# Kernel tuning notes

Hardware: AMD Instinct MI355X
Metric: run time of the kernel (lower is better)

## Reference

```python
import jax, jax.numpy as jnp
import numpy as np

N_NODES = 20000
N_EDGES = 640000
NODE_NF = 64
HIDDEN = 256
N_LAYERS = 4


def _linear_init(key, fan_in, fan_out, layers=None):
    shape = (fan_in, fan_out) if layers is None else (layers, fan_in, fan_out)
    scale = 1.0 / np.sqrt(fan_in)
    return jax.random.normal(key, shape, dtype=jnp.float32) * scale


def setup_inputs() -> dict:
    key = jax.random.key(0)
    ks = jax.random.split(key, 16)
    L, H = N_LAYERS, HIDDEN
    return {
        "h": jax.random.normal(ks[0], (N_NODES, NODE_NF), dtype=jnp.float32),
        "edge_index": jax.random.randint(ks[1], (2, N_EDGES), 0, N_NODES, dtype=jnp.int64),
        "coord_diff": jax.random.normal(ks[2], (N_EDGES, 3), dtype=jnp.float32),
        # embedding in / out
        "w_in": _linear_init(ks[3], NODE_NF, H),
        "b_in": jnp.zeros((H,), jnp.float32),
        "w_out": _linear_init(ks[4], H, NODE_NF),
        "b_out": jnp.zeros((NODE_NF,), jnp.float32),
        # per-layer edge MLP: Linear(2H+1 -> H), silu, Linear(H -> H), silu
        "edge_w1": _linear_init(ks[5], 2 * H + 1, H, L),
        "edge_b1": jnp.zeros((L, H), jnp.float32),
        "edge_w2": _linear_init(ks[6], H, H, L),
        "edge_b2": jnp.zeros((L, H), jnp.float32),
        # per-layer node MLP: Linear(2H -> H), silu, Linear(H -> H)
        "node_w1": _linear_init(ks[7], 2 * H, H, L),
        "node_b1": jnp.zeros((L, H), jnp.float32),
        "node_w2": _linear_init(ks[8], H, H, L),
        "node_b2": jnp.zeros((L, H), jnp.float32),
    }


def reference(h, edge_index, coord_diff, w_in, b_in, w_out, b_out,
              edge_w1, edge_b1, edge_w2, edge_b2,
              node_w1, node_b1, node_w2, node_b2):
    row, col = edge_index[0], edge_index[1]
    # radial is layer-independent: [E, 1]
    radial = jnp.sum(coord_diff ** 2, axis=1, keepdims=True)

    h = h @ w_in + b_in  # [N, H]
    n_nodes = h.shape[0]

    for l in range(N_LAYERS):
        # edge model: gather endpoints, concat with radial, 2-layer MLP
        m = jnp.concatenate([h[row], h[col], radial], axis=1)  # [E, 2H+1]
        m = jax.nn.silu(m @ edge_w1[l] + edge_b1[l])
        m = jax.nn.silu(m @ edge_w2[l] + edge_b2[l])  # [E, H]
        # node model: segment-sum aggregate over row, concat, 2-layer MLP
        agg = jax.ops.segment_sum(m, row, num_segments=n_nodes)  # [N, H]
        x = jnp.concatenate([h, agg], axis=1)  # [N, 2H]
        x = jax.nn.silu(x @ node_w1[l] + node_b1[l])
        h = x @ node_w2[l] + node_b2[l]  # recurrent=False: no residual

    return h @ w_out + b_out  # [N, node_nf]
```

## Files before the change

### kernel.cpp

```cpp
#include <hip/hip_runtime.h>
#include <hip/hip_bf16.h>
#include <cstdint>
#include <cstddef>

#define NN 20000
#define NE 640000
#define NF 64
#define HD 256
#define NL 4
#define HTS 640

typedef __attribute__((ext_vector_type(8))) short short8;
typedef __attribute__((ext_vector_type(4))) float f32x4;
typedef __attribute__((ext_vector_type(2))) float f32x2;

__device__ __forceinline__ float bf2f(unsigned short u){
  union { unsigned int i; float f; } x; x.i = ((unsigned int)u) << 16; return x.f;
}
__device__ __forceinline__ unsigned short f2bf(float f){
  union { float f; unsigned int i; } x; x.f = f;
  unsigned int r = x.i + 0x7FFFu + ((x.i >> 16) & 1u);
  return (unsigned short)(r >> 16);
}
__device__ __forceinline__ unsigned int pk2bf(float a, float b){
  union { __hip_bfloat162 h; unsigned int u; } cv;
  cv.h = __float22bfloat162_rn(float2{a, b});
  return cv.u;
}
__device__ __forceinline__ float silu_f(float v){
  float e = __builtin_amdgcn_exp2f(v * -1.442695041f);
  return v * __builtin_amdgcn_rcpf(1.0f + e);
}
__device__ __forceinline__ f32x2 silu2(f32x2 v){
  f32x2 t = v * (f32x2){-1.442695041f, -1.442695041f};
  f32x2 e = (f32x2){__builtin_amdgcn_exp2f(t.x), __builtin_amdgcn_exp2f(t.y)};
  f32x2 d = e + (f32x2){1.0f, 1.0f};
  f32x2 r = (f32x2){__builtin_amdgcn_rcpf(d.x), __builtin_amdgcn_rcpf(d.y)};
  return v * r;
}
__device__ __forceinline__ void async16(const void* g, void* l){
  __builtin_amdgcn_global_load_lds(
      (const __attribute__((address_space(1))) unsigned int*)g,
      (__attribute__((address_space(3))) unsigned int*)l, 16, 0, 0);
}

__global__ __launch_bounds__(256) void prep_small(
    const float* __restrict__ w_in, const float* __restrict__ w_out,
    const float* __restrict__ ew1, const float* __restrict__ ew2,
    const float* __restrict__ nw1, const float* __restrict__ nw2,
    const float* __restrict__ eb1,
    unsigned short* __restrict__ w_in_t, unsigned short* __restrict__ w_out_t,
    unsigned short* __restrict__ ew1cat, float* __restrict__ w1r,
    float* __restrict__ b1e,
    unsigned short* __restrict__ ew2t, unsigned short* __restrict__ nw1t,
    unsigned short* __restrict__ nw2t)
{
  const int s = blockIdx.y;
  const int tid = blockIdx.x * 256 + threadIdx.x;
  if (s == 18) {
    if (tid < NL * 512) {
      int l = tid >> 9, c = tid & 511;
      b1e[tid] = (c < 256) ? eb1[l * HD + c] : 0.0f;
    }
    return;
  }
  if (s >= 2 && s < 6) {
    int l = s - 2;
    if (tid >= 513 * HD) return;
    int k = tid / HD, n = tid - k * HD;
    float v = ew1[(size_t)l * 513 * HD + tid];
    if (k == 512) { w1r[l * HD + n] = v; return; }
    unsigned short* dst = ew1cat + (size_t)l * 512 * 256;
    if (k < 256) dst[(size_t)n * 256 + k] = f2bf(v);
    else         dst[(size_t)(256 + n) * 256 + (k - 256)] = f2bf(v);
    return;
  }
  const float* src; unsigned short* dst; int K, N;
  if (s == 0)      { src = w_in;  dst = w_in_t;  K = NF;   N = HD; }
  else if (s == 1) { src = w_out; dst = w_out_t; K = HD;   N = NF; }
  else if (s < 10) { int l = s-6;  src = ew2 + (size_t)l*HD*HD;   dst = ew2t + (size_t)l*HD*HD;  K = HD;   N = HD; }
  else if (s < 14) { int l = s-10; src = nw1 + (size_t)l*2*HD*HD; dst = nw1t + (size_t)l*HD*512; K = 2*HD; N = HD; }
  else             { int l = s-14; src = nw2 + (size_t)l*HD*HD;   dst = nw2t + (size_t)l*HD*HD;  K = HD;   N = HD; }
  if (tid >= K * N) return;
  int k = tid / N, n = tid - k * N;
  dst[(size_t)n * K + k] = f2bf(src[tid]);
}

__global__ __launch_bounds__(256) void prep_big(
    const float* __restrict__ h_in, const float* __restrict__ cd,
    unsigned short* __restrict__ hb_in, float* __restrict__ radial)
{
  const int s = blockIdx.y;
  const int tid = blockIdx.x * 256 + threadIdx.x;
  if (s == 0) {
    if (tid < NN * NF) hb_in[tid] = f2bf(h_in[tid]);
  } else {
    if (tid < NE) {
      float x = cd[tid*3+0], y = cd[tid*3+1], z = cd[tid*3+2];
      radial[tid] = x*x + y*y + z*z;
    }
  }
}

__global__ __launch_bounds__(256) void hist_k(const int* __restrict__ erow, int* __restrict__ hist){
  int e = blockIdx.x * 256 + threadIdx.x;
  if (e < NE){
    unsigned r = (unsigned)erow[e]; if (r >= NN) r = 0;
    atomicAdd(&hist[r], 1);
  }
}

__global__ __launch_bounds__(256) void scan_k(const int* __restrict__ hist,
                                              int* __restrict__ starts, int* __restrict__ cursor){
  __shared__ int part[256];
  const int t = threadIdx.x;
  const int CH = 79;
  int lo = t * CH, hi = lo + CH; if (hi > NN) hi = NN; if (lo > NN) lo = NN;
  int s = 0;
  for (int i = lo; i < hi; ++i) s += hist[i];
  part[t] = s; __syncthreads();
  for (int off = 1; off < 256; off <<= 1){
    int v = (t >= off) ? part[t - off] : 0;
    __syncthreads();
    part[t] += v;
    __syncthreads();
  }
  int base = (t == 0) ? 0 : part[t - 1];
  for (int i = lo; i < hi; ++i){ starts[i] = base; cursor[i] = base; base += hist[i]; }
  if (t == 255) starts[NN] = part[255];
}

__global__ __launch_bounds__(256) void scatter_k(const int* __restrict__ erow,
                                                 const int* __restrict__ ecol,
                                                 const float* __restrict__ radial,
                                                 int* __restrict__ cursor,
                                                 int* __restrict__ rowcol,
                                                 float* __restrict__ radial_s){
  int e = blockIdx.x * 256 + threadIdx.x;
  if (e < NE){
    unsigned r = (unsigned)erow[e]; if (r >= NN) r = 0;
    unsigned c = (unsigned)ecol[e]; if (c >= NN) c = 0;
    int pos = atomicAdd(&cursor[r], 1);
    rowcol[2*pos]   = (int)r;
    rowcol[2*pos+1] = (int)c;
    radial_s[pos] = radial[e];
  }
}

__global__ __launch_bounds__(256, 4) void node0_k(
    const unsigned short* __restrict__ hb,
    const unsigned short* __restrict__ w_in_t,
    const float* __restrict__ b_in,
    const unsigned short* __restrict__ w1cat0,
    const float* __restrict__ b1e0,
    unsigned short* __restrict__ hcur,
    unsigned short* __restrict__ hT,
    int M)
{
  __shared__ __align__(16) unsigned short As[32*64];
  __shared__ __align__(16) unsigned short Bs[256*32];
  __shared__ __align__(16) unsigned short xL[8*32*32];
  const int t = threadIdx.x;
  const int lane = t & 63, wave = t >> 6;
  const int ln15 = lane & 15, q = lane >> 4;
  const int bm = blockIdx.x;
  const int sc = (t & 3) * 8;
  const int srB = t >> 2;

  float bvin[4];
  #pragma unroll
  for (int j = 0; j < 4; ++j) bvin[j] = b_in[wave*64 + j*16 + ln15];

  f32x4 acc[2][4];
  #pragma unroll
  for (int i = 0; i < 2; ++i)
    #pragma unroll
    for (int j = 0; j < 4; ++j) acc[i][j] = (f32x4){0.f,0.f,0.f,0.f};

  async16(hb + (size_t)(bm*32 + (t >> 3)) * NF + (t & 7)*8, &As[t*8]);

  for (int kt = 0; kt < 2; ++kt) {
    #pragma unroll
    for (int i = 0; i < 4; ++i)
      async16(w_in_t + (size_t)(i*64 + srB) * NF + kt*32 + sc, &Bs[i*2048 + t*8]);
    __syncthreads();
    short8 fa[2], fb[4];
    #pragma unroll
    for (int i = 0; i < 2; ++i) fa[i] = *(const short8*)&As[(i*16 + ln15)*64 + kt*32 + q*8];
    #pragma unroll
    for (int j = 0; j < 4; ++j) fb[j] = *(const short8*)&Bs[(wave*64 + j*16 + ln15)*32 + q*8];
    #pragma unroll
    for (int i = 0; i < 2; ++i)
      #pragma unroll
      for (int j = 0; j < 4; ++j)
        acc[i][j] = __builtin_amdgcn_mfma_f32_16x16x32_bf16(fa[i], fb[j], acc[i][j], 0, 0, 0);
    __syncthreads();
  }

  #pragma unroll
  for (int i = 0; i < 2; ++i) {
    #pragma unroll
    for (int j = 0; j < 4; ++j) {
      const int n = wave*64 + j*16 + ln15;
      const int kt2 = n >> 5, k31 = n & 31;
      const int r0 = i*16 + q*4;
      const int m0 = bm*32 + r0;
      #pragma unroll
      for (int r = 0; r < 4; ++r) {
        unsigned short h = f2bf(acc[i][j][r] + bvin[j]);
        hcur[(size_t)(m0 + r) * HD + n] = h;
        xL[kt2*1024 + (r0 + r)*32 + k31] = h;
      }
    }
  }

  #pragma unroll
  for (int half = 0; half < 2; ++half) {
    #pragma unroll
    for (int i = 0; i < 2; ++i)
      #pragma unroll
      for (int j = 0; j < 4; ++j) acc[i][j] = (f32x4){0.f,0.f,0.f,0.f};
    for (int kt2 = 0; kt2 < 8; ++kt2) {
      #pragma unroll
      for (int i = 0; i < 4; ++i)
        async16(w1cat0 + (size_t)(half*256 + i*64 + srB) * 256 + kt2*32 + sc,
                &Bs[i*2048 + t*8]);
      __syncthreads();
      short8 fa[2], fb[4];
      #pragma unroll
      for (int i = 0; i < 2; ++i) fa[i] = *(const short8*)&xL[kt2*1024 + (i*16 + ln15)*32 + q*8];
      #pragma unroll
      for (int j = 0; j < 4; ++j) fb[j] = *(const short8*)&Bs[(wave*64 + j*16 + ln15)*32 + q*8];
      #pragma unroll
      for (int i = 0; i < 2; ++i)
        #pragma unroll
        for (int j = 0; j < 4; ++j)
          acc[i][j] = __builtin_amdgcn_mfma_f32_16x16x32_bf16(fa[i], fb[j], acc[i][j], 0, 0, 0);
      __syncthreads();
    }
    #pragma unroll
    for (int i = 0; i < 2; ++i) {
      #pragma unroll
      for (int j = 0; j < 4; ++j) {
        const int n = half*256 + wave*64 + j*16 + ln15;
        const float bv = b1e0[n];
        #pragma unroll
        for (int r = 0; r < 4; ++r) {
          const int m = bm*32 + i*16 + q*4 + r;
          hT[(size_t)m * HTS + n] = f2bf(acc[i][j][r] + bv);
        }
      }
    }
  }
  (void)M;
}

__global__ __launch_bounds__(256, 4) void node_k(
    unsigned short* __restrict__ hcur,
    float* __restrict__ aggF,
    const unsigned short* __restrict__ w1t,
    const float* __restrict__ b1,
    const unsigned short* __restrict__ w2t,
    const float* __restrict__ b2,
    const unsigned short* __restrict__ w1cat_next,
    const float* __restrict__ b1e_next,
    unsigned short* __restrict__ hT,
    const unsigned short* __restrict__ w_out_t,
    const float* __restrict__ b_out,
    float* __restrict__ outF,
    int M)
{
  __shared__ __align__(16) unsigned short As[32*32];
  __shared__ __align__(16) unsigned short Bs[256*32];
  __shared__ __align__(16) unsigned short xL[8*32*32];
  const int t = threadIdx.x;
  const int lane = t & 63, wave = t >> 6;
  const int ln15 = lane & 15, q = lane >> 4;
  const int bm = blockIdx.x;
  const int sc = (t & 3) * 8;
  const int srA = (t & 127) >> 2;
  const int srB = t >> 2;

  const int rowA = bm*32 + srA;
  const unsigned short* aSrc = hcur + (size_t)rowA * HD + sc;
  float* gSrc = aggF + (size_t)rowA * HD + sc;

  float bv1[4], bv2[4];
  #pragma unroll
  for (int j = 0; j < 4; ++j) {
    bv1[j] = b1[wave*64 + j*16 + ln15];
    bv2[j] = b2[wave*64 + j*16 + ln15];
  }

  f32x4 acc[2][4];
  #pragma unroll
  for (int i = 0; i < 2; ++i)
    #pragma unroll
    for (int j = 0; j < 4; ++j) acc[i][j] = (f32x4){0.f,0.f,0.f,0.f};

  for (int kt = 0; kt < 16; ++kt) {
    if (t < 128) {
      if (kt < 8) {
        async16(aSrc + kt*32, &As[t*8]);
      } else {
        float* p = gSrc + (kt-8)*32;
        float4 a0 = *(const float4*)p;
        float4 a1 = *(const float4*)(p + 4);
        union { unsigned int u[4]; short8 s8; } cv;
        cv.u[0] = pk2bf(a0.x, a0.y); cv.u[1] = pk2bf(a0.z, a0.w);
        cv.u[2] = pk2bf(a1.x, a1.y); cv.u[3] = pk2bf(a1.z, a1.w);
        *(float4*)p = float4{0.f,0.f,0.f,0.f};
        *(float4*)(p + 4) = float4{0.f,0.f,0.f,0.f};
        *(short8*)&As[t*8] = cv.s8;
      }
    }
    #pragma unroll
    for (int i = 0; i < 4; ++i)
      async16(w1t + (size_t)(i*64 + srB) * 512 + kt*32 + sc, &Bs[i*2048 + t*8]);
    __syncthreads();
    short8 fa[2], fb[4];
    #pragma unroll
    for (int i = 0; i < 2; ++i) fa[i] = *(const short8*)&As[(i*16 + ln15)*32 + q*8];
    #pragma unroll
    for (int j = 0; j < 4; ++j) fb[j] = *(const short8*)&Bs[(wave*64 + j*16 + ln15)*32 + q*8];
    #pragma unroll
    for (int i = 0; i < 2; ++i)
      #pragma unroll
      for (int j = 0; j < 4; ++j)
        acc[i][j] = __builtin_amdgcn_mfma_f32_16x16x32_bf16(fa[i], fb[j], acc[i][j], 0, 0, 0);
    __syncthreads();
  }

  #pragma unroll
  for (int i = 0; i < 2; ++i) {
    #pragma unroll
    for (int j = 0; j < 4; ++j) {
      const int k = wave*64 + j*16 + ln15;
      const int kt2 = k >> 5, k31 = k & 31;
      const f32x2 bb = (f32x2){bv1[j], bv1[j]};
      f32x2 s01 = (f32x2){acc[i][j][0], acc[i][j][1]} + bb;
      f32x2 s23 = (f32x2){acc[i][j][2], acc[i][j][3]} + bb;
      f32x2 r01 = silu2(s01);
      f32x2 r23 = silu2(s23);
      const int r0 = i*16 + q*4;
      xL[kt2*1024 + (r0  )*32 + k31] = f2bf(r01.x);
      xL[kt2*1024 + (r0+1)*32 + k31] = f2bf(r01.y);
      xL[kt2*1024 + (r0+2)*32 + k31] = f2bf(r23.x);
      xL[kt2*1024 + (r0+3)*32 + k31] = f2bf(r23.y);
    }
  }
  #pragma unroll
  for (int i = 0; i < 2; ++i)
    #pragma unroll
    for (int j = 0; j < 4; ++j) acc[i][j] = (f32x4){0.f,0.f,0.f,0.f};

  for (int kt2 = 0; kt2 < 8; ++kt2) {
    #pragma unroll
    for (int i = 0; i < 4; ++i)
      async16(w2t + (size_t)(i*64 + srB) * 256 + kt2*32 + sc, &Bs[i*2048 + t*8]);
    __syncthreads();
    short8 fa[2], fb[4];
    #pragma unroll
    for (int i = 0; i < 2; ++i) fa[i] = *(const short8*)&xL[kt2*1024 + (i*16 + ln15)*32 + q*8];
    #pragma unroll
    for (int j = 0; j < 4; ++j) fb[j] = *(const short8*)&Bs[(wave*64 + j*16 + ln15)*32 + q*8];
    #pragma unroll
    for (int i = 0; i < 2; ++i)
      #pragma unroll
      for (int j = 0; j < 4; ++j)
        acc[i][j] = __builtin_amdgcn_mfma_f32_16x16x32_bf16(fa[i], fb[j], acc[i][j], 0, 0, 0);
    __syncthreads();
  }

  #pragma unroll
  for (int i = 0; i < 2; ++i) {
    #pragma unroll
    for (int j = 0; j < 4; ++j) {
      const int n = wave*64 + j*16 + ln15;
      const int kt2 = n >> 5, k31 = n & 31;
      const int r0 = i*16 + q*4;
      const int m0 = bm*32 + r0;
      #pragma unroll
      for (int r = 0; r < 4; ++r) {
        unsigned short h = f2bf(acc[i][j][r] + bv2[j]);
        hcur[(size_t)(m0 + r) * HD + n] = h;
        xL[kt2*1024 + (r0 + r)*32 + k31] = h;
      }
    }
  }

  if (w1cat_next) {
    #pragma unroll
    for (int half = 0; half < 2; ++half) {
      #pragma unroll
      for (int i = 0; i < 2; ++i)
        #pragma unroll
        for (int j = 0; j < 4; ++j) acc[i][j] = (f32x4){0.f,0.f,0.f,0.f};
      for (int kt2 = 0; kt2 < 8; ++kt2) {
        #pragma unroll
        for (int i = 0; i < 4; ++i)
          async16(w1cat_next + (size_t)(half*256 + i*64 + srB) * 256 + kt2*32 + sc,
                  &Bs[i*2048 + t*8]);
        __syncthreads();
        short8 fa[2], fb[4];
        #pragma unroll
        for (int i = 0; i < 2; ++i) fa[i] = *(const short8*)&xL[kt2*1024 + (i*16 + ln15)*32 + q*8];
        #pragma unroll
        for (int j = 0; j < 4; ++j) fb[j] = *(const short8*)&Bs[(wave*64 + j*16 + ln15)*32 + q*8];
        #pragma unroll
        for (int i = 0; i < 2; ++i)
          #pragma unroll
          for (int j = 0; j < 4; ++j)
            acc[i][j] = __builtin_amdgcn_mfma_f32_16x16x32_bf16(fa[i], fb[j], acc[i][j], 0, 0, 0);
        __syncthreads();
      }
      #pragma unroll
      for (int i = 0; i < 2; ++i) {
        #pragma unroll
        for (int j = 0; j < 4; ++j) {
          const int n = half*256 + wave*64 + j*16 + ln15;
          const float bv = b1e_next[n];
          #pragma unroll
          for (int r = 0; r < 4; ++r) {
            const int m = bm*32 + i*16 + q*4 + r;
            hT[(size_t)m * HTS + n] = f2bf(acc[i][j][r] + bv);
          }
        }
      }
    }
  } else {
    const int nD = wave*16 + ln15;
    const float bvD = b_out[nD];
    f32x4 accD[2];
    accD[0] = (f32x4){0.f,0.f,0.f,0.f};
    accD[1] = (f32x4){0.f,0.f,0.f,0.f};
    for (int kt2 = 0; kt2 < 8; ++kt2) {
      async16(w_out_t + (size_t)srB * 256 + kt2*32 + sc, &Bs[t*8]);
      __syncthreads();
      short8 fa[2], fb;
      #pragma unroll
      for (int i = 0; i < 2; ++i) fa[i] = *(const short8*)&xL[kt2*1024 + (i*16 + ln15)*32 + q*8];
      fb = *(const short8*)&Bs[nD*32 + q*8];
      #pragma unroll
      for (int i = 0; i < 2; ++i)
        accD[i] = __builtin_amdgcn_mfma_f32_16x16x32_bf16(fa[i], fb, accD[i], 0, 0, 0);
      __syncthreads();
    }
    #pragma unroll
    for (int i = 0; i < 2; ++i) {
      #pragma unroll
      for (int r = 0; r < 4; ++r) {
        const int m = bm*32 + i*16 + q*4 + r;
        outF[(size_t)m * NF + nD] = accD[i][r] + bvD;
      }
    }
  }
  (void)M;
}

__global__ __launch_bounds__(256, 4) void edge_k(
    const unsigned short* __restrict__ hT,
    const int* __restrict__ rowcol,
    const float* __restrict__ radial_s,
    const float* __restrict__ w1r,
    const unsigned short* __restrict__ w2t,
    const float* __restrict__ b2,
    float* __restrict__ agg)
{
  __shared__ __align__(16) unsigned short MBUF[16896];
  __shared__ int   rowS[64];
  __shared__ float w1rS[256];
  unsigned short* M1  = MBUF;
  unsigned short* m2T = MBUF;

  const int t = threadIdx.x;
  const int lane = t & 63, wave = t >> 6;
  const int ln15 = lane & 15, q = lane >> 4;
  int blk = blockIdx.x;
  blk = (blk & 7) * ((int)gridDim.x >> 3) + (blk >> 3);
  const int e0 = blk * 64;
  const int sr = t >> 2;
  const int sc_swz = (((t & 3) ^ ((sr >> 1) & 3))) * 8;
  const int xq = ((q ^ ((ln15 >> 1) & 3))) * 8;

  const int2 rc = *(const int2*)(rowcol + 2*(e0 + sr));
  int rowv = 0;
  if (t < 64) rowv = rowcol[2*(e0 + t)];
  const float w1v = w1r[t];
  const float rad = radial_s[e0 + sr];

  float bv2[4];
  #pragma unroll
  for (int j = 0; j < 4; ++j) bv2[j] = b2[wave*64 + j*16 + ln15];

  const unsigned short* hr = hT + (size_t)rc.x * HTS + sc_swz;
  const unsigned short* hc = hT + (size_t)rc.y * HTS + 256 + sc_swz;

  short8 va[8], vb[8];
  #pragma unroll
  for (int ch = 0; ch < 8; ++ch) {
    va[ch] = *(const short8*)(hr + ch*32);
    vb[ch] = *(const short8*)(hc + ch*32);
  }

  if (t < 64) rowS[t] = rowv;
  w1rS[t] = w1v;

  const unsigned short* w2row[4];
  #pragma unroll
  for (int j = 0; j < 4; ++j)
    w2row[j] = w2t + (size_t)(wave*64 + j*16 + ln15) * HD + q*8;

  __syncthreads();

  const f32x2 rad2 = (f32x2){rad, rad};
  #pragma unroll
  for (int ch = 0; ch < 8; ++ch) {
    const int c0 = ch*32 + sc_swz;
    const unsigned int* ua = (const unsigned int*)&va[ch];
    const unsigned int* ub = (const unsigned int*)&vb[ch];
    union { unsigned int u[4]; short8 s; } res;
    #pragma unroll
    for (int i = 0; i < 4; ++i) {
      union { unsigned int i; float f; } alo, ahi, blo, bhi;
      alo.i = ua[i] << 16; ahi.i = ua[i] & 0xFFFF0000u;
      blo.i = ub[i] << 16; bhi.i = ub[i] & 0xFFFF0000u;
      f32x2 av = (f32x2){alo.f, ahi.f};
      f32x2 bv = (f32x2){blo.f, bhi.f};
      f32x2 wv = *(const f32x2*)&w1rS[c0 + 2*i];
      f32x2 o = av + bv;
      o = o + rad2 * wv;
      f32x2 sv = silu2(o);
      res.u[i] = pk2bf(sv.x, sv.y);
    }
    *(short8*)&M1[ch*2048 + sr*32 + (t & 3)*8] = res.s;
  }
  __syncthreads();

  f32x4 acc2[4][4];
  #pragma unroll
  for (int i = 0; i < 4; ++i)
    #pragma unroll
    for (int j = 0; j < 4; ++j) acc2[i][j] = (f32x4){0.f,0.f,0.f,0.f};

  __builtin_amdgcn_s_setprio(1);
  #pragma unroll
  for (int kt = 0; kt < 8; ++kt) {
    short8 fa[4], fb[4];
    #pragma unroll
    for (int j = 0; j < 4; ++j) fb[j] = *(const short8*)(w2row[j] + kt*32);
    #pragma unroll
    for (int i = 0; i < 4; ++i) fa[i] = *(const short8*)&M1[kt*2048 + (i*16 + ln15)*32 + xq];
    #pragma unroll
    for (int i = 0; i < 4; ++i)
      #pragma unroll
      for (int j = 0; j < 4; ++j)
        acc2[i][j] = __builtin_amdgcn_mfma_f32_16x16x32_bf16(fa[i], fb[j], acc2[i][j], 0, 0, 0);
  }
  __builtin_amdgcn_s_setprio(0);
  __syncthreads();

  #pragma unroll
  for (int i = 0; i < 4; ++i) {
    #pragma unroll
    for (int j = 0; j < 4; ++j) {
      const int n = wave*64 + j*16 + ln15;
      const f32x2 b2v = (f32x2){bv2[j], bv2[j]};
      f32x2 s01 = (f32x2){acc2[i][j][0], acc2[i][j][1]} + b2v;
      f32x2 s23 = (f32x2){acc2[i][j][2], acc2[i][j][3]} + b2v;
      f32x2 r01 = silu2(s01);
      f32x2 r23 = silu2(s23);
      const int m = i*16 + q*4;
      *(unsigned int*)&m2T[n*66 + m]     = pk2bf(r01.x, r01.y);
      *(unsigned int*)&m2T[n*66 + m + 2] = pk2bf(r23.x, r23.y);
    }
  }
  __syncthreads();

  {
    const int c = t;
    int cur = __builtin_amdgcn_readfirstlane(rowS[0]);
    float s = 0.f;
    #pragma unroll
    for (int m = 0; m < 64; m += 4) {
      unsigned int u0 = *(const unsigned int*)&m2T[c*66 + m];
      unsigned int u1 = *(const unsigned int*)&m2T[c*66 + m + 2];
      int n0 = __builtin_amdgcn_readfirstlane(rowS[m]);
      int n1 = __builtin_amdgcn_readfirstlane(rowS[m+1]);
      int n2 = __builtin_amdgcn_readfirstlane(rowS[m+2]);
      int n3 = __builtin_amdgcn_readfirstlane(rowS[m+3]);
      float f0 = bf2f((unsigned short)u0), f1 = bf2f((unsigned short)(u0 >> 16));
      float f2v = bf2f((unsigned short)u1), f3 = bf2f((unsigned short)(u1 >> 16));
      if (n0 != cur) { atomicAdd(&agg[(size_t)cur * HD + c], s); s = 0.f; cur = n0; }
      s += f0;
      if (n1 != cur) { atomicAdd(&agg[(size_t)cur * HD + c], s); s = 0.f; cur = n1; }
      s += f1;
      if (n2 != cur) { atomicAdd(&agg[(size_t)cur * HD + c], s); s = 0.f; cur = n2; }
      s += f2v;
      if (n3 != cur) { atomicAdd(&agg[(size_t)cur * HD + c], s); s = 0.f; cur = n3; }
      s += f3;
    }
    atomicAdd(&agg[(size_t)cur * HD + c], s);
  }
}

extern "C" void kernel_launch(void* const* d_in, const int* in_sizes, int n_in,
                              void* d_out, int out_size, void* d_ws, size_t ws_size,
                              hipStream_t stream)
{
  (void)in_sizes; (void)n_in; (void)out_size; (void)ws_size;
  const float* h_in  = (const float*)d_in[0];
  const int*   ei    = (const int*)d_in[1];
  const float* cd    = (const float*)d_in[2];
  const float* w_in  = (const float*)d_in[3];
  const float* b_in  = (const float*)d_in[4];
  const float* w_out = (const float*)d_in[5];
  const float* b_out = (const float*)d_in[6];
  const float* ew1   = (const float*)d_in[7];
  const float* eb1   = (const float*)d_in[8];
  const float* ew2   = (const float*)d_in[9];
  const float* eb2   = (const float*)d_in[10];
  const float* nw1   = (const float*)d_in[11];
  const float* nb1   = (const float*)d_in[12];
  const float* nw2   = (const float*)d_in[13];
  const float* nb2   = (const float*)d_in[14];
  float* out = (float*)d_out;

  char* base = (char*)d_ws;
  size_t off = 0;
  auto WS = [&](size_t bytes) -> char* {
    char* p = base + off;
    off = (off + bytes + 255) & ~(size_t)255;
    return p;
  };
  float*          radial  = (float*)WS((size_t)NE * 4);
  unsigned short* hb_in   = (unsigned short*)WS((size_t)NN * NF * 2);
  unsigned short* hcur    = (unsigned short*)WS((size_t)NN * HD * 2);
  float*          aggF    = (float*)WS((size_t)NN * HD * 4);
  unsigned short* hT      = (unsigned short*)WS((size_t)NN * HTS * 2);
  unsigned short* w_in_t  = (unsigned short*)WS((size_t)NF * HD * 2);
  unsigned short* w_out_t = (unsigned short*)WS((size_t)NF * HD * 2);
  unsigned short* ew1cat  = (unsigned short*)WS((size_t)NL * 512 * 256 * 2);
  float*          w1r     = (float*)WS((size_t)NL * HD * 4);
  float*          b1e     = (float*)WS((size_t)NL * 512 * 4);
  unsigned short* ew2t    = (unsigned short*)WS((size_t)NL * HD * HD * 2);
  unsigned short* nw1t    = (unsigned short*)WS((size_t)NL * HD * 512 * 2);
  unsigned short* nw2t    = (unsigned short*)WS((size_t)NL * HD * HD * 2);
  int*            hist    = (int*)WS((size_t)NN * 4);
  int*            starts  = (int*)WS((size_t)(NN + 1) * 4);
  int*            cursor  = (int*)WS((size_t)NN * 4);
  int*            rowcol  = (int*)WS((size_t)NE * 2 * 4);
  float*          radial_s= (float*)WS((size_t)NE * 4);

  hipMemsetAsync(hist, 0, (size_t)NN * 4, stream);
  hipMemsetAsync(aggF, 0, (size_t)NN * HD * 4, stream);
  prep_small<<<dim3(513, 19), 256, 0, stream>>>(w_in, w_out, ew1, ew2, nw1, nw2, eb1,
      w_in_t, w_out_t, ew1cat, w1r, b1e, ew2t, nw1t, nw2t);
  prep_big<<<dim3(5000, 2), 256, 0, stream>>>(h_in, cd, hb_in, radial);
  hist_k<<<NE / 256, 256, 0, stream>>>(ei, hist);
  scan_k<<<1, 256, 0, stream>>>(hist, starts, cursor);
  scatter_k<<<NE / 256, 256, 0, stream>>>(ei, ei + NE, radial, cursor, rowcol, radial_s);

  node0_k<<<NN / 32, 256, 0, stream>>>(hb_in, w_in_t, b_in, ew1cat, b1e, hcur, hT, NN);

  for (int l = 0; l < NL; ++l) {
    edge_k<<<NE / 64, 256, 0, stream>>>(hT, rowcol, radial_s,
        w1r + l * HD, ew2t + (size_t)l * HD * HD, eb2 + l * HD, aggF);
    const int last = (l == NL - 1);
    node_k<<<NN / 32, 256, 0, stream>>>(hcur, aggF,
        nw1t + (size_t)l * HD * 512, nb1 + l * HD,
        nw2t + (size_t)l * HD * HD, nb2 + l * HD,
        last ? nullptr : (ew1cat + (size_t)(l+1) * 512 * 256),
        last ? nullptr : (b1e + (size_t)(l+1) * 512),
        hT, w_out_t, b_out, out, NN);
  }
}
```

Measured before the change: 1.146 ms.

## Halve node-kernel row tile to 16 and parallelize the CSR prefix scan

The node kernels (node0_k, node_k) now process 16 rows per block instead of 32, doubling the grid from 625 to 1250 blocks so more CUs stay busy on the 20000-node GEMMs. The price is that each block reloads the full weight tiles for half as many rows, which doubles weight traffic from L2. The single-block serial histogram scan is replaced by a three-kernel block-parallel scan (block sums, scan of sums, per-block scan). This removes a long serial step but adds two launches.

```diff
diff --git a/kernel.cpp b/kernel.cpp
--- a/kernel.cpp
+++ b/kernel.cpp
@@ -9,6 +9,8 @@
 #define HD 256
 #define NL 4
 #define HTS 640
+#define SR 16
+#define NB 79
 
 typedef __attribute__((ext_vector_type(8))) short short8;
 typedef __attribute__((ext_vector_type(4))) float f32x4;
@@ -110,24 +112,50 @@
   }
 }
 
-__global__ __launch_bounds__(256) void scan_k(const int* __restrict__ hist,
-                                              int* __restrict__ starts, int* __restrict__ cursor){
+__global__ __launch_bounds__(256) void scan1_k(const int* __restrict__ hist, int* __restrict__ bsum){
+  __shared__ int red[256];
+  const int t = threadIdx.x;
+  const int bin = blockIdx.x * 256 + t;
+  red[t] = (bin < NN) ? hist[bin] : 0;
+  __syncthreads();
+  for (int off = 128; off > 0; off >>= 1){
+    if (t < off) red[t] += red[t + off];
+    __syncthreads();
+  }
+  if (t == 0) bsum[blockIdx.x] = red[0];
+}
+
+__global__ __launch_bounds__(256) void scan2_k(const int* __restrict__ bsum, int* __restrict__ boff){
   __shared__ int part[256];
   const int t = threadIdx.x;
-  const int CH = 79;
-  int lo = t * CH, hi = lo + CH; if (hi > NN) hi = NN; if (lo > NN) lo = NN;
-  int s = 0;
-  for (int i = lo; i < hi; ++i) s += hist[i];
-  part[t] = s; __syncthreads();
+  int v = (t < NB) ? bsum[t] : 0;
+  part[t] = v;
+  __syncthreads();
   for (int off = 1; off < 256; off <<= 1){
-    int v = (t >= off) ? part[t - off] : 0;
-    __syncthreads();
-    part[t] += v;
-    __syncthreads();
-  }
-  int base = (t == 0) ? 0 : part[t - 1];
-  for (int i = lo; i < hi; ++i){ starts[i] = base; cursor[i] = base; base += hist[i]; }
-  if (t == 255) starts[NN] = part[255];
+    int p = (t >= off) ? part[t - off] : 0;
+    __syncthreads();
+    part[t] += p;
+    __syncthreads();
+  }
+  if (t < NB) boff[t] = part[t] - v;
+}
+
+__global__ __launch_bounds__(256) void scan3_k(const int* __restrict__ hist,
+                                               const int* __restrict__ boff,
+                                               int* __restrict__ cursor){
+  __shared__ int part[256];
+  const int t = threadIdx.x;
+  const int bin = blockIdx.x * 256 + t;
+  int v = (bin < NN) ? hist[bin] : 0;
+  part[t] = v;
+  __syncthreads();
+  for (int off = 1; off < 256; off <<= 1){
+    int p = (t >= off) ? part[t - off] : 0;
+    __syncthreads();
+    part[t] += p;
+    __syncthreads();
+  }
+  if (bin < NN) cursor[bin] = boff[blockIdx.x] + part[t] - v;
 }
 
 __global__ __launch_bounds__(256) void scatter_k(const int* __restrict__ erow,
@@ -154,12 +182,11 @@
     const unsigned short* __restrict__ w1cat0,
     const float* __restrict__ b1e0,
     unsigned short* __restrict__ hcur,
-    unsigned short* __restrict__ hT,
-    int M)
+    unsigned short* __restrict__ hT)
 {
-  __shared__ __align__(16) unsigned short As[32*64];
+  __shared__ __align__(16) unsigned short As[SR*64];
   __shared__ __align__(16) unsigned short Bs[256*32];
-  __shared__ __align__(16) unsigned short xL[8*32*32];
+  __shared__ __align__(16) unsigned short xL[8*SR*32];
   const int t = threadIdx.x;
   const int lane = t & 63, wave = t >> 6;
   const int ln15 = lane & 15, q = lane >> 4;
@@ -171,88 +198,72 @@
   #pragma unroll
   for (int j = 0; j < 4; ++j) bvin[j] = b_in[wave*64 + j*16 + ln15];
 
-  f32x4 acc[2][4];
-  #pragma unroll
-  for (int i = 0; i < 2; ++i)
-    #pragma unroll
-    for (int j = 0; j < 4; ++j) acc[i][j] = (f32x4){0.f,0.f,0.f,0.f};
-
-  async16(hb + (size_t)(bm*32 + (t >> 3)) * NF + (t & 7)*8, &As[t*8]);
+  f32x4 acc[4];
+  #pragma unroll
+  for (int j = 0; j < 4; ++j) acc[j] = (f32x4){0.f,0.f,0.f,0.f};
+
+  if (t < 128)
+    async16(hb + (size_t)(bm*SR + (t >> 3)) * NF + (t & 7)*8, &As[t*8]);
 
   for (int kt = 0; kt < 2; ++kt) {
     #pragma unroll
     for (int i = 0; i < 4; ++i)
       async16(w_in_t + (size_t)(i*64 + srB) * NF + kt*32 + sc, &Bs[i*2048 + t*8]);
     __syncthreads();
-    short8 fa[2], fb[4];
-    #pragma unroll
-    for (int i = 0; i < 2; ++i) fa[i] = *(const short8*)&As[(i*16 + ln15)*64 + kt*32 + q*8];
+    short8 fa, fb[4];
+    fa = *(const short8*)&As[ln15*64 + kt*32 + q*8];
     #pragma unroll
     for (int j = 0; j < 4; ++j) fb[j] = *(const short8*)&Bs[(wave*64 + j*16 + ln15)*32 + q*8];
     #pragma unroll
-    for (int i = 0; i < 2; ++i)
-      #pragma unroll
-      for (int j = 0; j < 4; ++j)
-        acc[i][j] = __builtin_amdgcn_mfma_f32_16x16x32_bf16(fa[i], fb[j], acc[i][j], 0, 0, 0);
-    __syncthreads();
-  }
-
-  #pragma unroll
-  for (int i = 0; i < 2; ++i) {
-    #pragma unroll
-    for (int j = 0; j < 4; ++j) {
-      const int n = wave*64 + j*16 + ln15;
-      const int kt2 = n >> 5, k31 = n & 31;
-      const int r0 = i*16 + q*4;
-      const int m0 = bm*32 + r0;
-      #pragma unroll
-      for (int r = 0; r < 4; ++r) {
-        unsigned short h = f2bf(acc[i][j][r] + bvin[j]);
-        hcur[(size_t)(m0 + r) * HD + n] = h;
-        xL[kt2*1024 + (r0 + r)*32 + k31] = h;
-      }
+    for (int j = 0; j < 4; ++j)
+      acc[j] = __builtin_amdgcn_mfma_f32_16x16x32_bf16(fa, fb[j], acc[j], 0, 0, 0);
+    __syncthreads();
+  }
+
+  #pragma unroll
+  for (int j = 0; j < 4; ++j) {
+    const int n = wave*64 + j*16 + ln15;
+    const int kt2 = n >> 5, k31 = n & 31;
+    const int r0 = q*4;
+    const int m0 = bm*SR + r0;
+    #pragma unroll
+    for (int r = 0; r < 4; ++r) {
+      unsigned short h = f2bf(acc[j][r] + bvin[j]);
+      hcur[(size_t)(m0 + r) * HD + n] = h;
+      xL[kt2*512 + (r0 + r)*32 + k31] = h;
     }
   }
 
   #pragma unroll
   for (int half = 0; half < 2; ++half) {
     #pragma unroll
-    for (int i = 0; i < 2; ++i)
-      #pragma unroll
-      for (int j = 0; j < 4; ++j) acc[i][j] = (f32x4){0.f,0.f,0.f,0.f};
+    for (int j = 0; j < 4; ++j) acc[j] = (f32x4){0.f,0.f,0.f,0.f};
     for (int kt2 = 0; kt2 < 8; ++kt2) {
       #pragma unroll
       for (int i = 0; i < 4; ++i)
         async16(w1cat0 + (size_t)(half*256 + i*64 + srB) * 256 + kt2*32 + sc,
                 &Bs[i*2048 + t*8]);
       __syncthreads();
-      short8 fa[2], fb[4];
-      #pragma unroll
-      for (int i = 0; i < 2; ++i) fa[i] = *(const short8*)&xL[kt2*1024 + (i*16 + ln15)*32 + q*8];
+      short8 fa, fb[4];
+      fa = *(const short8*)&xL[kt2*512 + ln15*32 + q*8];
       #pragma unroll
       for (int j = 0; j < 4; ++j) fb[j] = *(const short8*)&Bs[(wave*64 + j*16 + ln15)*32 + q*8];
       #pragma unroll
-      for (int i = 0; i < 2; ++i)
-        #pragma unroll
-        for (int j = 0; j < 4; ++j)
-          acc[i][j] = __builtin_amdgcn_mfma_f32_16x16x32_bf16(fa[i], fb[j], acc[i][j], 0, 0, 0);
+      for (int j = 0; j < 4; ++j)
+        acc[j] = __builtin_amdgcn_mfma_f32_16x16x32_bf16(fa, fb[j], acc[j], 0, 0, 0);
       __syncthreads();
     }
     #pragma unroll
-    for (int i = 0; i < 2; ++i) {
+    for (int j = 0; j < 4; ++j) {
+      const int n = half*256 + wave*64 + j*16 + ln15;
+      const float bv = b1e0[n];
       #pragma unroll
-      for (int j = 0; j < 4; ++j) {
-        const int n = half*256 + wave*64 + j*16 + ln15;
-        const float bv = b1e0[n];
-        #pragma unroll
-        for (int r = 0; r < 4; ++r) {
-          const int m = bm*32 + i*16 + q*4 + r;
-          hT[(size_t)m * HTS + n] = f2bf(acc[i][j][r] + bv);
-        }
+      for (int r = 0; r < 4; ++r) {
+        const int m = bm*SR + q*4 + r;
+        hT[(size_t)m * HTS + n] = f2bf(acc[j][r] + bv);
       }
     }
   }
-  (void)M;
 }
 
 __global__ __launch_bounds__(256, 4) void node_k(
@@ -267,21 +278,20 @@
     unsigned short* __restrict__ hT,
     const unsigned short* __restrict__ w_out_t,
     const float* __restrict__ b_out,
-    float* __restrict__ outF,
-    int M)
+    float* __restrict__ outF)
 {
-  __shared__ __align__(16) unsigned short As[32*32];
+  __shared__ __align__(16) unsigned short As[SR*32];
   __shared__ __align__(16) unsigned short Bs[256*32];
-  __shared__ __align__(16) unsigned short xL[8*32*32];
+  __shared__ __align__(16) unsigned short xL[8*SR*32];
   const int t = threadIdx.x;
   const int lane = t & 63, wave = t >> 6;
   const int ln15 = lane & 15, q = lane >> 4;
   const int bm = blockIdx.x;
   const int sc = (t & 3) * 8;
-  const int srA = (t & 127) >> 2;
+  const int srA = (t & 63) >> 2;
   const int srB = t >> 2;
 
-  const int rowA = bm*32 + srA;
+  const int rowA = bm*SR + srA;
   const unsigned short* aSrc = hcur + (size_t)rowA * HD + sc;
   float* gSrc = aggF + (size_t)rowA * HD + sc;
 
@@ -292,14 +302,12 @@
     bv2[j] = b2[wave*64 + j*16 + ln15];
   }
 
-  f32x4 acc[2][4];
-  #pragma unroll
-  for (int i = 0; i < 2; ++i)
-    #pragma unroll
-    for (int j = 0; j < 4; ++j) acc[i][j] = (f32x4){0.f,0.f,0.f,0.f};
+  f32x4 acc[4];
+  #pragma unroll
+  for (int j = 0; j < 4; ++j) acc[j] = (f32x4){0.f,0.f,0.f,0.f};
 
   for (int kt = 0; kt < 16; ++kt) {
-    if (t < 128) {
+    if (t < 64) {
       if (kt < 8) {
         async16(aSrc + kt*32, &As[t*8]);
       } else {
@@ -318,74 +326,60 @@
     for (int i = 0; i < 4; ++i)
       async16(w1t + (size_t)(i*64 + srB) * 512 + kt*32 + sc, &Bs[i*2048 + t*8]);
     __syncthreads();
-    short8 fa[2], fb[4];
-    #pragma unroll
-    for (int i = 0; i < 2; ++i) fa[i] = *(const short8*)&As[(i*16 + ln15)*32 + q*8];
+    short8 fa, fb[4];
+    fa = *(const short8*)&As[ln15*32 + q*8];
     #pragma unroll
     for (int j = 0; j < 4; ++j) fb[j] = *(const short8*)&Bs[(wave*64 + j*16 + ln15)*32 + q*8];
     #pragma unroll
-    for (int i = 0; i < 2; ++i)
-      #pragma unroll
-      for (int j = 0; j < 4; ++j)
-        acc[i][j] = __builtin_amdgcn_mfma_f32_16x16x32_bf16(fa[i], fb[j], acc[i][j], 0, 0, 0);
-    __syncthreads();
-  }
-
-  #pragma unroll
-  for (int i = 0; i < 2; ++i) {
-    #pragma unroll
-    for (int j = 0; j < 4; ++j) {
-      const int k = wave*64 + j*16 + ln15;
-      const int kt2 = k >> 5, k31 = k & 31;
-      const f32x2 bb = (f32x2){bv1[j], bv1[j]};
-      f32x2 s01 = (f32x2){acc[i][j][0], acc[i][j][1]} + bb;
-      f32x2 s23 = (f32x2){acc[i][j][2], acc[i][j][3]} + bb;
-      f32x2 r01 = silu2(s01);
-      f32x2 r23 = silu2(s23);
-      const int r0 = i*16 + q*4;
-      xL[kt2*1024 + (r0  )*32 + k31] = f2bf(r01.x);
-      xL[kt2*1024 + (r0+1)*32 + k31] = f2bf(r01.y);
-      xL[kt2*1024 + (r0+2)*32 + k31] = f2bf(r23.x);
-      xL[kt2*1024 + (r0+3)*32 + k31] = f2bf(r23.y);
-    }
-  }
-  #pragma unroll
-  for (int i = 0; i < 2; ++i)
-    #pragma unroll
-    for (int j = 0; j < 4; ++j) acc[i][j] = (f32x4){0.f,0.f,0.f,0.f};
+    for (int j = 0; j < 4; ++j)
+      acc[j] = __builtin_amdgcn_mfma_f32_16x16x32_bf16(fa, fb[j], acc[j], 0, 0, 0);
+    __syncthreads();
+  }
+
+  #pragma unroll
+  for (int j = 0; j < 4; ++j) {
+    const int k = wave*64 + j*16 + ln15;
+    const int kt2 = k >> 5, k31 = k & 31;
+    const f32x2 bb = (f32x2){bv1[j], bv1[j]};
+    f32x2 s01 = (f32x2){acc[j][0], acc[j][1]} + bb;
+    f32x2 s23 = (f32x2){acc[j][2], acc[j][3]} + bb;
+    f32x2 r01 = silu2(s01);
+    f32x2 r23 = silu2(s23);
+    const int r0 = q*4;
+    xL[kt2*512 + (r0  )*32 + k31] = f2bf(r01.x);
+    xL[kt2*512 + (r0+1)*32 + k31] = f2bf(r01.y);
+    xL[kt2*512 + (r0+2)*32 + k31] = f2bf(r23.x);
+    xL[kt2*512 + (r0+3)*32 + k31] = f2bf(r23.y);
+  }
+  #pragma unroll
+  for (int j = 0; j < 4; ++j) acc[j] = (f32x4){0.f,0.f,0.f,0.f};
 
   for (int kt2 = 0; kt2 < 8; ++kt2) {
     #pragma unroll
     for (int i = 0; i < 4; ++i)
       async16(w2t + (size_t)(i*64 + srB) * 256 + kt2*32 + sc, &Bs[i*2048 + t*8]);
     __syncthreads();
-    short8 fa[2], fb[4];
-    #pragma unroll
-    for (int i = 0; i < 2; ++i) fa[i] = *(const short8*)&xL[kt2*1024 + (i*16 + ln15)*32 + q*8];
+    short8 fa, fb[4];
+    fa = *(const short8*)&xL[kt2*512 + ln15*32 + q*8];
     #pragma unroll
     for (int j = 0; j < 4; ++j) fb[j] = *(const short8*)&Bs[(wave*64 + j*16 + ln15)*32 + q*8];
     #pragma unroll
-    for (int i = 0; i < 2; ++i)
-      #pragma unroll
-      for (int j = 0; j < 4; ++j)
-        acc[i][j] = __builtin_amdgcn_mfma_f32_16x16x32_bf16(fa[i], fb[j], acc[i][j], 0, 0, 0);
-    __syncthreads();
-  }
-
-  #pragma unroll
-  for (int i = 0; i < 2; ++i) {
-    #pragma unroll
-    for (int j = 0; j < 4; ++j) {
-      const int n = wave*64 + j*16 + ln15;
-      const int kt2 = n >> 5, k31 = n & 31;
-      const int r0 = i*16 + q*4;
-      const int m0 = bm*32 + r0;
-      #pragma unroll
-      for (int r = 0; r < 4; ++r) {
-        unsigned short h = f2bf(acc[i][j][r] + bv2[j]);
-        hcur[(size_t)(m0 + r) * HD + n] = h;
-        xL[kt2*1024 + (r0 + r)*32 + k31] = h;
-      }
+    for (int j = 0; j < 4; ++j)
+      acc[j] = __builtin_amdgcn_mfma_f32_16x16x32_bf16(fa, fb[j], acc[j], 0, 0, 0);
+    __syncthreads();
+  }
+
+  #pragma unroll
+  for (int j = 0; j < 4; ++j) {
+    const int n = wave*64 + j*16 + ln15;
+    const int kt2 = n >> 5, k31 = n & 31;
+    const int r0 = q*4;
+    const int m0 = bm*SR + r0;
+    #pragma unroll
+    for (int r = 0; r < 4; ++r) {
+      unsigned short h = f2bf(acc[j][r] + bv2[j]);
+      hcur[(size_t)(m0 + r) * HD + n] = h;
+      xL[kt2*512 + (r0 + r)*32 + k31] = h;
     }
   }
 
@@ -393,69 +387,51 @@
     #pragma unroll
     for (int half = 0; half < 2; ++half) {
       #pragma unroll
-      for (int i = 0; i < 2; ++i)
-        #pragma unroll
-        for (int j = 0; j < 4; ++j) acc[i][j] = (f32x4){0.f,0.f,0.f,0.f};
+      for (int j = 0; j < 4; ++j) acc[j] = (f32x4){0.f,0.f,0.f,0.f};
       for (int kt2 = 0; kt2 < 8; ++kt2) {
         #pragma unroll
         for (int i = 0; i < 4; ++i)
           async16(w1cat_next + (size_t)(half*256 + i*64 + srB) * 256 + kt2*32 + sc,
                   &Bs[i*2048 + t*8]);
         __syncthreads();
-        short8 fa[2], fb[4];
-        #pragma unroll
-        for (int i = 0; i < 2; ++i) fa[i] = *(const short8*)&xL[kt2*1024 + (i*16 + ln15)*32 + q*8];
+        short8 fa, fb[4];
+        fa = *(const short8*)&xL[kt2*512 + ln15*32 + q*8];
         #pragma unroll
         for (int j = 0; j < 4; ++j) fb[j] = *(const short8*)&Bs[(wave*64 + j*16 + ln15)*32 + q*8];
         #pragma unroll
-        for (int i = 0; i < 2; ++i)
-          #pragma unroll
-          for (int j = 0; j < 4; ++j)
-            acc[i][j] = __builtin_amdgcn_mfma_f32_16x16x32_bf16(fa[i], fb[j], acc[i][j], 0, 0, 0);
+        for (int j = 0; j < 4; ++j)
+          acc[j] = __builtin_amdgcn_mfma_f32_16x16x32_bf16(fa, fb[j], acc[j], 0, 0, 0);
         __syncthreads();
       }
       #pragma unroll
-      for (int i = 0; i < 2; ++i) {
+      for (int j = 0; j < 4; ++j) {
+        const int n = half*256 + wave*64 + j*16 + ln15;
+        const float bv = b1e_next[n];
         #pragma unroll
-        for (int j = 0; j < 4; ++j) {
-          const int n = half*256 + wave*64 + j*16 + ln15;
-          const float bv = b1e_next[n];
-          #pragma unroll
-          for (int r = 0; r < 4; ++r) {
-            const int m = bm*32 + i*16 + q*4 + r;
-            hT[(size_t)m * HTS + n] = f2bf(acc[i][j][r] + bv);
-          }
+        for (int r = 0; r < 4; ++r) {
+          const int m = bm*SR + q*4 + r;
+          hT[(size_t)m * HTS + n] = f2bf(acc[j][r] + bv);
         }
       }
     }
   } else {
     const int nD = wave*16 + ln15;
     const float bvD = b_out[nD];
-    f32x4 accD[2];
-    accD[0] = (f32x4){0.f,0.f,0.f,0.f};
-    accD[1] = (f32x4){0.f,0.f,0.f,0.f};
+    f32x4 accD = (f32x4){0.f,0.f,0.f,0.f};
     for (int kt2 = 0; kt2 < 8; ++kt2) {
       async16(w_out_t + (size_t)srB * 256 + kt2*32 + sc, &Bs[t*8]);
       __syncthreads();
-      short8 fa[2], fb;
-      #pragma unroll
-      for (int i = 0; i < 2; ++i) fa[i] = *(const short8*)&xL[kt2*1024 + (i*16 + ln15)*32 + q*8];
-      fb = *(const short8*)&Bs[nD*32 + q*8];
-      #pragma unroll
-      for (int i = 0; i < 2; ++i)
-        accD[i] = __builtin_amdgcn_mfma_f32_16x16x32_bf16(fa[i], fb, accD[i], 0, 0, 0);
+      short8 fa = *(const short8*)&xL[kt2*512 + ln15*32 + q*8];
+      short8 fb = *(const short8*)&Bs[nD*32 + q*8];
+      accD = __builtin_amdgcn_mfma_f32_16x16x32_bf16(fa, fb, accD, 0, 0, 0);
       __syncthreads();
     }
     #pragma unroll
-    for (int i = 0; i < 2; ++i) {
-      #pragma unroll
-      for (int r = 0; r < 4; ++r) {
-        const int m = bm*32 + i*16 + q*4 + r;
-        outF[(size_t)m * NF + nD] = accD[i][r] + bvD;
-      }
-    }
-  }
-  (void)M;
+    for (int r = 0; r < 4; ++r) {
+      const int m = bm*SR + q*4 + r;
+      outF[(size_t)m * NF + nD] = accD[r] + bvD;
+    }
+  }
 }
 
 __global__ __launch_bounds__(256, 4) void edge_k(
@@ -647,7 +623,8 @@
   unsigned short* nw1t    = (unsigned short*)WS((size_t)NL * HD * 512 * 2);
   unsigned short* nw2t    = (unsigned short*)WS((size_t)NL * HD * HD * 2);
   int*            hist    = (int*)WS((size_t)NN * 4);
-  int*            starts  = (int*)WS((size_t)(NN + 1) * 4);
+  int*            bsum    = (int*)WS((size_t)128 * 4);
+  int*            boff    = (int*)WS((size_t)128 * 4);
   int*            cursor  = (int*)WS((size_t)NN * 4);
   int*            rowcol  = (int*)WS((size_t)NE * 2 * 4);
   float*          radial_s= (float*)WS((size_t)NE * 4);
@@ -658,20 +635,22 @@
       w_in_t, w_out_t, ew1cat, w1r, b1e, ew2t, nw1t, nw2t);
   prep_big<<<dim3(5000, 2), 256, 0, stream>>>(h_in, cd, hb_in, radial);
   hist_k<<<NE / 256, 256, 0, stream>>>(ei, hist);
-  scan_k<<<1, 256, 0, stream>>>(hist, starts, cursor);
+  scan1_k<<<NB, 256, 0, stream>>>(hist, bsum);
+  scan2_k<<<1, 256, 0, stream>>>(bsum, boff);
+  scan3_k<<<NB, 256, 0, stream>>>(hist, boff, cursor);
   scatter_k<<<NE / 256, 256, 0, stream>>>(ei, ei + NE, radial, cursor, rowcol, radial_s);
 
-  node0_k<<<NN / 32, 256, 0, stream>>>(hb_in, w_in_t, b_in, ew1cat, b1e, hcur, hT, NN);
+  node0_k<<<NN / SR, 256, 0, stream>>>(hb_in, w_in_t, b_in, ew1cat, b1e, hcur, hT);
 
   for (int l = 0; l < NL; ++l) {
     edge_k<<<NE / 64, 256, 0, stream>>>(hT, rowcol, radial_s,
         w1r + l * HD, ew2t + (size_t)l * HD * HD, eb2 + l * HD, aggF);
     const int last = (l == NL - 1);
-    node_k<<<NN / 32, 256, 0, stream>>>(hcur, aggF,
+    node_k<<<NN / SR, 256, 0, stream>>>(hcur, aggF,
         nw1t + (size_t)l * HD * 512, nb1 + l * HD,
         nw2t + (size_t)l * HD * HD, nb2 + l * HD,
         last ? nullptr : (ew1cat + (size_t)(l+1) * 512 * 256),
         last ? nullptr : (b1e + (size_t)(l+1) * 512),
-        hT, w_out_t, b_out, out, NN);
-  }
-}
+        hT, w_out_t, b_out, out);
+  }
+}
```

After: 1.181 ms. 3.1% more time.
